# Optimization experiments

Measured on AMD Instinct MI355X. Metric: run time of the kernel, lower is better.

The kernel has to match this reference:

```python
import jax, jax.numpy as jnp
import numpy as np

N, E = 50000, 800000
IN, H, D, C = 128, 4, 32, 40   # in_feats, heads, num_hiddens, n_classes
SLOPE, EPS = 0.2, 1e-5


def _glorot(key, shape, fan_in):
    return jax.random.normal(key, shape, dtype=jnp.float32) * (1.0 / np.sqrt(fan_in))


def setup_inputs() -> dict:
    key = jax.random.key(0)
    ks = jax.random.split(key, 24)
    inp = {
        "feat": jax.random.normal(ks[0], (N, IN), dtype=jnp.float32),
        "src": jax.random.randint(ks[1], (E,), 0, N, dtype=jnp.int32),
        "dst": jax.random.randint(ks[2], (E,), 0, N, dtype=jnp.int32),
    }
    # layer dims: (in_hidden, out_hidden)
    dims = [(IN, D), (H * D, D), (H * D, C)]
    k = 3
    for i, (fin, fout) in enumerate(dims):
        inp[f"Wc{i}"] = _glorot(ks[k], (fin, H * fout), fin); k += 1
        inp[f"al{i}"] = _glorot(ks[k], (H, fout), fout); k += 1
        inp[f"ar{i}"] = _glorot(ks[k], (H, fout), fout); k += 1
        inp[f"bc{i}"] = jnp.zeros((H * fout,), dtype=jnp.float32)
        inp[f"Wl{i}"] = _glorot(ks[k], (fin, H * fout), fin); k += 1
    for i in range(2):  # BN after layers 0 and 1
        inp[f"g{i}"] = jnp.ones((H * D,), dtype=jnp.float32)
        inp[f"b{i}"] = jnp.zeros((H * D,), dtype=jnp.float32)
    inp["bias_last"] = jnp.zeros((C,), dtype=jnp.float32)
    return inp


def _gat_layer(x, src, dst, Wc, al, ar, bc, Wl):
    n = x.shape[0]
    h, d = al.shape
    z = (x @ Wc).reshape(n, h, d)                      # [N,H,D]
    el = jnp.sum(z * al, axis=-1)                      # [N,H]
    er = jnp.sum(z * ar, axis=-1)                      # [N,H]
    e = jax.nn.leaky_relu(el[src] + er[dst], SLOPE)    # [E,H]
    m = jax.ops.segment_max(e, dst, num_segments=n)    # edge-softmax (stable)
    ex = jnp.exp(e - m[dst])
    s = jax.ops.segment_sum(ex, dst, num_segments=n)
    alpha = ex / jnp.where(s == 0, 1.0, s)[dst]        # [E,H]
    agg = jax.ops.segment_sum(alpha[:, :, None] * z[src], dst, num_segments=n)
    conv = agg + bc.reshape(h, d)
    lin = (x @ Wl).reshape(n, h, d)
    return conv + lin                                   # [N,H,D]


def _bn(x, g, b):
    mu = jnp.mean(x, axis=0)
    var = jnp.mean((x - mu) ** 2, axis=0)
    return (x - mu) * jax.lax.rsqrt(var + EPS) * g + b


def reference(feat, src, dst,
              Wc0, al0, ar0, bc0, Wl0,
              Wc1, al1, ar1, bc1, Wl1,
              Wc2, al2, ar2, bc2, Wl2,
              g0, b0, g1, b1, bias_last):
    h = feat
    h = _gat_layer(h, src, dst, Wc0, al0, ar0, bc0, Wl0)
    h = jax.nn.relu(_bn(h.reshape(h.shape[0], -1), g0, b0))
    h = _gat_layer(h, src, dst, Wc1, al1, ar1, bc1, Wl1)
    h = jax.nn.relu(_bn(h.reshape(h.shape[0], -1), g1, b1))
    h = _gat_layer(h, src, dst, Wc2, al2, ar2, bc2, Wl2)
    h = h.mean(axis=1)                                  # mean over heads -> [N,C]
    return h + bias_last
```

## Files before the change

### kernel.cpp

```cpp
#include <hip/hip_runtime.h>
#include <hip/hip_bf16.h>

typedef __hip_bfloat16 bf16;
typedef __attribute__((ext_vector_type(8))) short short8;
typedef __attribute__((ext_vector_type(4))) float f32x4;

__device__ __forceinline__ float b2f(bf16 x) { return __bfloat162float(x); }
__device__ __forceinline__ float bits2f(unsigned short u) {
    return __uint_as_float(((unsigned)u) << 16);
}
__device__ __forceinline__ float ldw(const void* p, int i, int m) {
    return m ? ((const float*)p)[i] : b2f(((const bf16*)p)[i]);
}

__global__ __launch_bounds__(256) void k_zero_probe(int* __restrict__ counts, float* __restrict__ bn0,
                                                    float* __restrict__ bn1, int n,
                                                    const void* __restrict__ feat, int* __restrict__ mode) {
    int t = blockIdx.x * 256 + threadIdx.x;
    if (t < n) counts[t] = 0;
    if (t < 256) { bn0[t] = 0.f; bn1[t] = 0.f; }
    if (blockIdx.x == 0 && threadIdx.x < 64) {
        const bf16* p = (const bf16*)feat;
        int lane = threadIdx.x;
        float m = 0.f;
        for (int i = lane; i < 2048; i += 64) {
            float v = fabsf(b2f(p[2 * i]));
            if (!(v < 1e30f)) v = 1e30f;
            m = fmaxf(m, v);
        }
        #pragma unroll
        for (int off = 32; off > 0; off >>= 1) m = fmaxf(m, __shfl_xor(m, off, 64));
        if (lane == 0) *mode = (m > 1e8f) ? 1 : 0;
    }
}

struct SmallDesc { const void* src; float* dst; int n; };
struct SmallArgs { SmallDesc d[14]; };
__global__ __launch_bounds__(256) void k_prep(const void* __restrict__ Wc0, const void* __restrict__ Wl0,
                                              const void* __restrict__ Wc1, const void* __restrict__ Wl1,
                                              const void* __restrict__ Wc2, const void* __restrict__ Wl2,
                                              bf16* __restrict__ Wt0, bf16* __restrict__ Wt1,
                                              bf16* __restrict__ Wt2, SmallArgs sa,
                                              const int* __restrict__ mode) {
    int m = *mode;
    int bx = blockIdx.x;
    if (bx < 416) {
        int t = bx * 256 + threadIdx.x;
        const void* Wc; const void* Wl; bf16* Wt; int HC, c2, k;
        if (t < 32768)       { Wc = Wc0; Wl = Wl0; Wt = Wt0; HC = 128; c2 = t & 255; k = t >> 8; }
        else if (t < 65536)  { t -= 32768; Wc = Wc1; Wl = Wl1; Wt = Wt1; HC = 128; c2 = t & 255; k = t >> 8; }
        else                 { t -= 65536; Wc = Wc2; Wl = Wl2; Wt = Wt2; HC = 160; c2 = t % 320; k = t / 320; }
        float v = (c2 < HC) ? ldw(Wc, k * HC + c2, m) : ldw(Wl, k * HC + c2 - HC, m);
        int tile = c2 >> 4, c16 = c2 & 15, kg = k >> 5, q = (k >> 3) & 3, j = k & 7;
        Wt[tile * 2048 + kg * 512 + c16 * 32 + q * 8 + j] = __float2bfloat16(v);
    } else {
        #pragma unroll 1
        for (int i = 0; i < 14; i++) {
            const SmallDesc sd = sa.d[i];
            for (int t = threadIdx.x; t < sd.n; t += 256) sd.dst[t] = ldw(sd.src, t, m);
        }
    }
}


__global__ __launch_bounds__(256) void k_hist(const int* __restrict__ dst, int* __restrict__ counts,
                                              int e, int rpb) {
    int range = blockIdx.x & 7;
    int t = (blockIdx.x >> 3) * 256 + threadIdx.x;
    if (t < e) {
        int d = dst[t];
        if ((int)((unsigned)d / (unsigned)rpb) == range) atomicAdd(&counts[d], 1);
    }
}

__global__ __launch_bounds__(1024) void k_scan(const int* __restrict__ counts, int* __restrict__ row_ptr,
                                               int* __restrict__ cursor, int n) {
    __shared__ int wsum[16];
    __shared__ int carry_s;
    int lane = threadIdx.x & 63, w = threadIdx.x >> 6;
    if (threadIdx.x == 0) carry_s = 0;
    __syncthreads();
    for (int base = 0; base < n; base += 16384) {
        int i0 = base + (int)threadIdx.x * 16;
        int v[16];
        #pragma unroll
        for (int jb = 0; jb < 16; jb += 4) {
            int idx = i0 + jb;
            if (idx + 3 < n) {
                int4 t4 = *(const int4*)(counts + idx);
                v[jb] = t4.x; v[jb + 1] = t4.y; v[jb + 2] = t4.z; v[jb + 3] = t4.w;
            } else {
                #pragma unroll
                for (int q = 0; q < 4; q++) v[jb + q] = (idx + q < n) ? counts[idx + q] : 0;
            }
        }
        int pre[16]; int tot = 0;
        #pragma unroll
        for (int j = 0; j < 16; j++) { pre[j] = tot; tot += v[j]; }
        int x = tot;
        #pragma unroll
        for (int off = 1; off < 64; off <<= 1) {
            int t = __shfl_up(x, off, 64);
            if (lane >= off) x += t;
        }
        if (lane == 63) wsum[w] = x;
        __syncthreads();
        if (w == 0 && lane < 16) {
            int s = wsum[lane];
            #pragma unroll
            for (int off = 1; off < 16; off <<= 1) {
                int t = __shfl_up(s, off, 64);
                if (lane >= off) s += t;
            }
            wsum[lane] = s;
        }
        __syncthreads();
        int carry = carry_s;
        int woff = (w == 0) ? 0 : wsum[w - 1];
        int excl = carry + woff + x - tot;
        #pragma unroll
        for (int jb = 0; jb < 16; jb += 4) {
            int idx = i0 + jb;
            if (idx + 3 < n) {
                int4 rp = {excl + pre[jb], excl + pre[jb + 1], excl + pre[jb + 2], excl + pre[jb + 3]};
                *(int4*)(row_ptr + idx) = rp;
                *(int4*)(cursor + idx) = rp;
            } else {
                #pragma unroll
                for (int q = 0; q < 4; q++)
                    if (idx + q < n) { row_ptr[idx + q] = excl + pre[jb + q]; cursor[idx + q] = excl + pre[jb + q]; }
            }
        }
        __syncthreads();
        if (threadIdx.x == 0) carry_s = carry + wsum[15];
        __syncthreads();
    }
    if (threadIdx.x == 0) row_ptr[n] = carry_s;
}

__global__ __launch_bounds__(256) void k_scatter(const int* __restrict__ src, const int* __restrict__ dst,
                                                 int* __restrict__ cursor, int* __restrict__ ssrc,
                                                 int e, int rpb) {
    int range = blockIdx.x & 7;
    int t = (blockIdx.x >> 3) * 256 + threadIdx.x;
    if (t < e) {
        int d = dst[t];
        if ((int)((unsigned)d / (unsigned)rpb) == range) {
            int idx = atomicAdd(&cursor[d], 1);
            ssrc[idx] = src[t];
        }
    }
}

template <int HC, int CT, int AMODE, bool FELR>
__global__ __launch_bounds__(256) void k_gemm_mfma(const void* __restrict__ Av, const int* __restrict__ mode,
                                                   const bf16* __restrict__ Wt,
                                                   bf16* __restrict__ Zh, float* __restrict__ Lin,
                                                   const float* __restrict__ alp, const float* __restrict__ arp,
                                                   float* __restrict__ elp, float* __restrict__ erp,
                                                   const float* __restrict__ bnsum, const float* __restrict__ bnsq,
                                                   const float* __restrict__ gg, const float* __restrict__ bb,
                                                   float invn, int n) {
    __shared__ short lds_a[64 * 136];
    __shared__ float lds_bn[256];
    int tid = threadIdx.x;
    int wv = tid >> 6, lane = tid & 63;
    int quad = lane >> 4, m16 = lane & 15;
    int row0 = blockIdx.x * 64 + wv * 16;
    int row0b = blockIdx.x * 64;
    int col0 = blockIdx.y * (CT * 16);
    if constexpr (AMODE == 2) {
        if (tid < 128) {
            float mu = bnsum[tid] * invn;
            float var = bnsq[tid] * invn - mu * mu;
            float sc = rsqrtf(var + 1e-5f) * gg[tid];
            lds_bn[tid] = sc;
            lds_bn[128 + tid] = bb[tid] - mu * sc;
        }
        __syncthreads();
    }
    bool af32 = false;
    if constexpr (AMODE == 1) af32 = (*mode != 0);
    #pragma unroll
    for (int i = 0; i < 4; i++) {
        int f = i * 256 + tid;
        int row = f >> 4, c8 = f & 15;
        int arow = row0b + row; if (arow >= n) arow = n - 1;
        union { bf16 h[8]; short8 s; } u;
        if (AMODE == 2 || (AMODE == 1 && af32)) {
            const float4* ap = (const float4*)((const float*)Av + (size_t)arow * 128 + c8 * 8);
            float4 g0v = ap[0], g1v = ap[1];
            float vals[8] = {g0v.x, g0v.y, g0v.z, g0v.w, g1v.x, g1v.y, g1v.z, g1v.w};
            if constexpr (AMODE == 2) {
                int c0 = c8 * 8;
                #pragma unroll
                for (int j = 0; j < 8; j++) {
                    float r = vals[j] * lds_bn[c0 + j] + lds_bn[128 + c0 + j];
                    vals[j] = r > 0.f ? r : 0.f;
                }
            }
            #pragma unroll
            for (int j = 0; j < 8; j++) u.h[j] = __float2bfloat16(vals[j]);
        } else {
            u.s = *(const short8*)((const bf16*)Av + (size_t)arow * 128 + c8 * 8);
        }
        *(short8*)(&lds_a[row * 136 + c8 * 8]) = u.s;
    }
    __syncthreads();
    f32x4 acc[CT] = {};
    const short8* Bp = (const short8*)Wt;
    int lr = wv * 16 + m16;
    int ctb = blockIdx.y * CT;
    #pragma unroll
    for (int k8 = 0; k8 < 16; k8 += 4) {
        short8 a = *(const short8*)(&lds_a[lr * 136 + (k8 + quad) * 8]);
        #pragma unroll
        for (int c = 0; c < CT; c++) {
            short8 b = Bp[(size_t)(ctb + c) * 256 + k8 * 16 + m16 * 4 + quad];
            acc[c] = __builtin_amdgcn_mfma_f32_16x16x32_bf16(a, b, acc[c], 0, 0, 0);
        }
    }
    if constexpr (FELR && HC == 128) {
        if (blockIdx.y == 0) {
            float a0[4], a1[4], r0[4], r1[4];
            #pragma unroll
            for (int h = 0; h < 4; h++) {
                a0[h] = alp[h * 32 + m16]; a1[h] = alp[h * 32 + 16 + m16];
                r0[h] = arp[h * 32 + m16]; r1[h] = arp[h * 32 + 16 + m16];
            }
            #pragma unroll
            for (int reg = 0; reg < 4; reg++) {
                float eh[8];
                #pragma unroll
                for (int h = 0; h < 4; h++) {
                    eh[h]     = acc[2 * h][reg] * a0[h] + acc[2 * h + 1][reg] * a1[h];
                    eh[4 + h] = acc[2 * h][reg] * r0[h] + acc[2 * h + 1][reg] * r1[h];
                }
                #pragma unroll
                for (int off = 1; off < 16; off <<= 1) {
                    #pragma unroll
                    for (int k = 0; k < 8; k++) eh[k] += __shfl_xor(eh[k], off, 64);
                }
                int r = row0 + quad * 4 + reg;
                float vl = (m16 & 2) ? ((m16 & 1) ? eh[3] : eh[2]) : ((m16 & 1) ? eh[1] : eh[0]);
                float vr = (m16 & 2) ? ((m16 & 1) ? eh[7] : eh[6]) : ((m16 & 1) ? eh[5] : eh[4]);
                if (r < n && m16 < 4) { elp[(size_t)r * 4 + m16] = vl; erp[(size_t)r * 4 + m16] = vr; }
            }
        }
    }
    if constexpr (FELR && HC == 160) {
        if (blockIdx.y == 0) {
            float alv[10], arv[10];
            #pragma unroll
            for (int c = 0; c < 10; c++) { alv[c] = alp[c * 16 + m16]; arv[c] = arp[c * 16 + m16]; }
            #pragma unroll
            for (int reg = 0; reg < 4; reg++) {
                float eh[8] = {0.f, 0.f, 0.f, 0.f, 0.f, 0.f, 0.f, 0.f};
                #pragma unroll
                for (int c = 0; c < 10; c++) {
                    int col = c * 16 + m16;
                    float zl = acc[c][reg] * alv[c];
                    float zr = acc[c][reg] * arv[c];
                    bool h0 = col < 40, h1 = (col >= 40) & (col < 80);
                    bool h2 = (col >= 80) & (col < 120), h3 = col >= 120;
                    eh[0] += h0 ? zl : 0.f; eh[1] += h1 ? zl : 0.f;
                    eh[2] += h2 ? zl : 0.f; eh[3] += h3 ? zl : 0.f;
                    eh[4] += h0 ? zr : 0.f; eh[5] += h1 ? zr : 0.f;
                    eh[6] += h2 ? zr : 0.f; eh[7] += h3 ? zr : 0.f;
                }
                #pragma unroll
                for (int off = 1; off < 16; off <<= 1) {
                    #pragma unroll
                    for (int k = 0; k < 8; k++) eh[k] += __shfl_xor(eh[k], off, 64);
                }
                int r = row0 + quad * 4 + reg;
                float vl = (m16 & 2) ? ((m16 & 1) ? eh[3] : eh[2]) : ((m16 & 1) ? eh[1] : eh[0]);
                float vr = (m16 & 2) ? ((m16 & 1) ? eh[7] : eh[6]) : ((m16 & 1) ? eh[5] : eh[4]);
                if (r < n && m16 < 4) { elp[(size_t)r * 4 + m16] = vl; erp[(size_t)r * 4 + m16] = vr; }
            }
        }
    }
    #pragma unroll
    for (int c = 0; c < CT; c++) {
        int gc = col0 + c * 16 + m16;
        #pragma unroll
        for (int reg = 0; reg < 4; reg++) {
            int r = row0 + quad * 4 + reg;
            if (r >= n) continue;
            float v = acc[c][reg];
            if (gc < HC) Zh[(size_t)r * HC + gc] = __float2bfloat16(v);
            else         Lin[(size_t)r * HC + gc - HC] = v;
        }
    }
}

template <int HC, int D, bool LAST>
__global__ __launch_bounds__(256, 8) void k_gather(const int* __restrict__ row_ptr, const int* __restrict__ ssrc,
                                                   const float* __restrict__ el, const float* __restrict__ er,
                                                   const float* __restrict__ bc, const bf16* __restrict__ Z,
                                                   float* __restrict__ Y, const float* __restrict__ bias,
                                                   float* __restrict__ out, int n) {
    constexpr int DPL = HC / 16;
    constexpr int UN = (DPL == 8) ? 4 : 2;
    int node = (int)((blockIdx.x * blockDim.x + threadIdx.x) >> 6);
    int lane = threadIdx.x & 63;
    if (node >= n) return;
    int qi = lane >> 4;
    int t16 = lane & 15;
    int hq = t16 >> 2;
    int beg = row_ptr[node], end = row_ptr[node + 1];
    float4 er4 = ((const float4*)er)[node];
    const float4* el4p = (const float4*)el;
    const bf16* Zt = Z + t16 * DPL;
    float acc[DPL];
    #pragma unroll
    for (int k = 0; k < DPL; k++) acc[k] = 0.f;
    float ss = 0.f;
    for (int base = beg; base < end; base += 64) {
        int idx = base + lane;
        bool valid = idx < end;
        int s_my = valid ? ssrc[idx] : 0;
        float4 e4 = el4p[s_my];
        float x0 = e4.x + er4.x; x0 = x0 > 0.f ? x0 : 0.2f * x0;
        float x1 = e4.y + er4.y; x1 = x1 > 0.f ? x1 : 0.2f * x1;
        float x2 = e4.z + er4.z; x2 = x2 > 0.f ? x2 : 0.2f * x2;
        float x3 = e4.w + er4.w; x3 = x3 > 0.f ? x3 : 0.2f * x3;
        float w0 = valid ? __expf(x0) : 0.f;
        float w1 = valid ? __expf(x1) : 0.f;
        float w2 = valid ? __expf(x2) : 0.f;
        float w3 = valid ? __expf(x3) : 0.f;
        int cnt = end - base; if (cnt > 64) cnt = 64;
        int iters = (cnt + 3) >> 2;
        for (int j = 0; j < iters; j += UN) {
            int sv[UN]; float gv[UN];
            #pragma unroll
            for (int f = 0; f < UN; f++) {
                int sl = qi + ((j + f) << 2);
                sv[f] = __shfl(s_my, sl, 64);
                float a0 = __shfl(w0, sl, 64);
                float a1 = __shfl(w1, sl, 64);
                float a2 = __shfl(w2, sl, 64);
                float a3 = __shfl(w3, sl, 64);
                gv[f] = (hq & 2) ? ((hq & 1) ? a3 : a2) : ((hq & 1) ? a1 : a0);
                ss += gv[f];
            }
            if constexpr (DPL == 8) {
                short8 z[UN];
                #pragma unroll
                for (int f = 0; f < UN; f++) z[f] = *(const short8*)(Zt + (size_t)sv[f] * HC);
                #pragma unroll
                for (int f = 0; f < UN; f++) {
                    #pragma unroll
                    for (int k = 0; k < 8; k++)
                        acc[k] += gv[f] * bits2f((unsigned short)z[f][k]);
                }
            } else {
                __hip_bfloat162 z[UN][DPL / 2];
                #pragma unroll
                for (int f = 0; f < UN; f++) {
                    const __hip_bfloat162* z2 = (const __hip_bfloat162*)(Zt + (size_t)sv[f] * HC);
                    #pragma unroll
                    for (int k2 = 0; k2 < DPL / 2; k2++) z[f][k2] = z2[k2];
                }
                #pragma unroll
                for (int f = 0; f < UN; f++) {
                    #pragma unroll
                    for (int k2 = 0; k2 < DPL / 2; k2++) {
                        acc[2 * k2]     += gv[f] * b2f(z[f][k2].x);
                        acc[2 * k2 + 1] += gv[f] * b2f(z[f][k2].y);
                    }
                }
            }
        }
    }
    #pragma unroll
    for (int k = 0; k < DPL; k++) {
        acc[k] += __shfl_xor(acc[k], 16, 64);
        acc[k] += __shfl_xor(acc[k], 32, 64);
    }
    ss += __shfl_xor(ss, 16, 64);
    ss += __shfl_xor(ss, 32, 64);
    float inv = (end > beg) ? 1.f / ss : 0.f;
    if constexpr (!LAST) {
        if ((lane & 48) == 0) {
            float* yr = Y + (size_t)node * HC + t16 * DPL;
            const float* bcr = bc + t16 * DPL;
            #pragma unroll
            for (int k = 0; k < DPL; k++) yr[k] += acc[k] * inv + bcr[k];
        }
    } else {
        float yv[DPL];
        const float* lr = Y + (size_t)node * HC + t16 * DPL;
        const float* bcr = bc + t16 * DPL;
        #pragma unroll
        for (int k = 0; k < DPL; k++) yv[k] = acc[k] * inv + bcr[k] + lr[k];
        #pragma unroll
        for (int k = 0; k < DPL; k++) {
            yv[k] += __shfl_xor(yv[k], 4, 64);
            yv[k] += __shfl_xor(yv[k], 8, 64);
        }
        if (lane < 4) {
            float* orow = out + (size_t)node * 40 + t16 * DPL;
            const float* br = bias + t16 * DPL;
            #pragma unroll
            for (int k = 0; k < DPL; k++) orow[k] = 0.25f * yv[k] + br[k];
        }
    }
}

__global__ __launch_bounds__(256) void k_bn_stats(const float* __restrict__ Y, float* __restrict__ sum,
                                                  float* __restrict__ sumsq, int n) {
    __shared__ float4 lds_s[8][32];
    __shared__ float4 lds_q[8][32];
    int t = threadIdx.x;
    int q = t & 31, g = t >> 5;
    const float4* Y4 = (const float4*)Y;
    float4 s = {0.f, 0.f, 0.f, 0.f}, ss = {0.f, 0.f, 0.f, 0.f};
    const int stride = 128 * 8;
    int r = blockIdx.x * 8 + g;
    for (; r + stride < n; r += 2 * stride) {
        float4 v0 = Y4[(size_t)r * 32 + q];
        float4 v1 = Y4[(size_t)(r + stride) * 32 + q];
        s.x += v0.x; s.y += v0.y; s.z += v0.z; s.w += v0.w;
        ss.x += v0.x * v0.x; ss.y += v0.y * v0.y; ss.z += v0.z * v0.z; ss.w += v0.w * v0.w;
        s.x += v1.x; s.y += v1.y; s.z += v1.z; s.w += v1.w;
        ss.x += v1.x * v1.x; ss.y += v1.y * v1.y; ss.z += v1.z * v1.z; ss.w += v1.w * v1.w;
    }
    if (r < n) {
        float4 v = Y4[(size_t)r * 32 + q];
        s.x += v.x; s.y += v.y; s.z += v.z; s.w += v.w;
        ss.x += v.x * v.x; ss.y += v.y * v.y; ss.z += v.z * v.z; ss.w += v.w * v.w;
    }
    lds_s[g][q] = s; lds_q[g][q] = ss;
    __syncthreads();
    if (t < 32) {
        float4 S = lds_s[0][t], Q = lds_q[0][t];
        #pragma unroll
        for (int g2 = 1; g2 < 8; g2++) {
            float4 a = lds_s[g2][t], b = lds_q[g2][t];
            S.x += a.x; S.y += a.y; S.z += a.z; S.w += a.w;
            Q.x += b.x; Q.y += b.y; Q.z += b.z; Q.w += b.w;
        }
        atomicAdd(&sum[4 * t + 0], S.x); atomicAdd(&sum[4 * t + 1], S.y);
        atomicAdd(&sum[4 * t + 2], S.z); atomicAdd(&sum[4 * t + 3], S.w);
        atomicAdd(&sumsq[4 * t + 0], Q.x); atomicAdd(&sumsq[4 * t + 1], Q.y);
        atomicAdd(&sumsq[4 * t + 2], Q.z); atomicAdd(&sumsq[4 * t + 3], Q.w);
    }
}


extern "C" void kernel_launch(void* const* d_in, const int* in_sizes, int n_in,
                              void* d_out, int out_size, void* d_ws, size_t ws_size,
                              hipStream_t stream) {
    (void)n_in; (void)out_size; (void)ws_size;
    const int N = in_sizes[0] / 128;
    const int E = in_sizes[1];

    const int* src = (const int*)d_in[1];
    const int* dst = (const int*)d_in[2];
    float* out = (float*)d_out;

    char* p = (char*)d_ws;
    auto carve = [&](size_t bytes) {
        void* q = (void*)p;
        p += (bytes + 255) & ~(size_t)255;
        return q;
    };
    int*   mode    = (int*)  carve(256);
    bf16*  zh      = (bf16*) carve((size_t)N * 160 * 2);
    float* P0      = (float*)carve((size_t)N * 160 * 4);
    float* P1      = (float*)carve((size_t)N * 128 * 4);
    float* el      = (float*)carve((size_t)N * 4 * 4);
    float* er      = (float*)carve((size_t)N * 4 * 4);
    float* bn0     = (float*)carve(256 * 4);
    float* bn1     = (float*)carve(256 * 4);
    int*   counts  = (int*)  carve((size_t)N * 4);
    int*   row_ptr = (int*)  carve((size_t)(N + 1) * 4);
    int*   cursor  = (int*)  carve((size_t)N * 4);
    int*   ssrc    = (int*)  carve((size_t)E * 4);
    bf16*  Wt0     = (bf16*) carve((size_t)2 * 128 * 128 * 2);
    bf16*  Wt1     = (bf16*) carve((size_t)2 * 128 * 128 * 2);
    bf16*  Wt2     = (bf16*) carve((size_t)2 * 160 * 128 * 2);
    const int small_idx[14] = {4, 5, 6, 9, 10, 11, 14, 15, 16, 18, 19, 20, 21, 22};
    float* Wsm[14];
    for (int j = 0; j < 14; j++) Wsm[j] = (float*)carve((size_t)in_sizes[small_idx[j]] * 4);

    const float* alw[3] = {Wsm[0], Wsm[3], Wsm[6]};
    const float* arw[3] = {Wsm[1], Wsm[4], Wsm[7]};
    const float* bcw[3] = {Wsm[2], Wsm[5], Wsm[8]};
    const float* g0 = Wsm[9];
    const float* b0 = Wsm[10];
    const float* g1 = Wsm[11];
    const float* b1 = Wsm[12];
    const float* bias_last = Wsm[13];

    const int EB = (E + 255) / 256;
    const int GB_ROWS = (N + 63) / 64;
    const int NODE_BLK = (N + 3) / 4;
    const float invn = 1.f / (float)N;
    const int RPB = (N + 7) / 8;

    k_zero_probe<<<(N + 255) / 256, 256, 0, stream>>>(counts, bn0, bn1, N, d_in[0], mode);
    SmallArgs sa;
    for (int j = 0; j < 14; j++) sa.d[j] = SmallDesc{d_in[small_idx[j]], Wsm[j], in_sizes[small_idx[j]]};
    k_prep<<<417, 256, 0, stream>>>(d_in[3], d_in[7], d_in[8], d_in[12], d_in[13], d_in[17],
                                    Wt0, Wt1, Wt2, sa, mode);
    k_hist<<<8 * EB, 256, 0, stream>>>(dst, counts, E, RPB);
    k_scan<<<1, 1024, 0, stream>>>(counts, row_ptr, cursor, N);
    k_scatter<<<8 * EB, 256, 0, stream>>>(src, dst, cursor, ssrc, E, RPB);

    k_gemm_mfma<128, 8, 1, true><<<dim3(GB_ROWS, 2), 256, 0, stream>>>(
        d_in[0], mode, Wt0, zh, P0, alw[0], arw[0], el, er,
        nullptr, nullptr, nullptr, nullptr, 0.f, N);
    k_gather<128, 32, false><<<NODE_BLK, 256, 0, stream>>>(row_ptr, ssrc, el, er, bcw[0], zh,
                                                           P0, nullptr, nullptr, N);
    k_bn_stats<<<128, 256, 0, stream>>>(P0, bn0, bn0 + 128, N);

    k_gemm_mfma<128, 8, 2, true><<<dim3(GB_ROWS, 2), 256, 0, stream>>>(
        P0, mode, Wt1, zh, P1, alw[1], arw[1], el, er,
        bn0, bn0 + 128, g0, b0, invn, N);
    k_gather<128, 32, false><<<NODE_BLK, 256, 0, stream>>>(row_ptr, ssrc, el, er, bcw[1], zh,
                                                           P1, nullptr, nullptr, N);
    k_bn_stats<<<128, 256, 0, stream>>>(P1, bn1, bn1 + 128, N);

    k_gemm_mfma<160, 10, 2, true><<<dim3(GB_ROWS, 2), 256, 0, stream>>>(
        P1, mode, Wt2, zh, P0, alw[2], arw[2], el, er,
        bn1, bn1 + 128, g1, b1, invn, N);
    k_gather<160, 40, true><<<NODE_BLK, 256, 0, stream>>>(row_ptr, ssrc, el, er, bcw[2], zh,
                                                          P0, bias_last, out, N);
}
```

Baseline: 468.6 us.

## Compute edge weights per lane in gather and simplify histogram to a single pass

The gather kernel no longer loads 64 edges per chunk cooperatively and broadcasts source ids and four per-head weights through shuffles. Each lane now loads its own source index and its own head's el value, then computes the leaky-relu and exp itself, which removes the five shuffles per edge. The cost is redundant ssrc/el loads and exp evaluations across the 16 lanes sharing an edge. The histogram kernel also drops its 8-way range partitioning, reading dst once with plain atomics, which trades atomic locality for one-eighth the launched blocks.

```diff
diff --git a/kernel.cpp b/kernel.cpp
--- a/kernel.cpp
+++ b/kernel.cpp
@@ -63,14 +63,9 @@
 }
 
 
-__global__ __launch_bounds__(256) void k_hist(const int* __restrict__ dst, int* __restrict__ counts,
-                                              int e, int rpb) {
-    int range = blockIdx.x & 7;
-    int t = (blockIdx.x >> 3) * 256 + threadIdx.x;
-    if (t < e) {
-        int d = dst[t];
-        if ((int)((unsigned)d / (unsigned)rpb) == range) atomicAdd(&counts[d], 1);
-    }
+__global__ __launch_bounds__(256) void k_hist(const int* __restrict__ dst, int* __restrict__ counts, int e) {
+    int t = blockIdx.x * 256 + threadIdx.x;
+    if (t < e) atomicAdd(&counts[dst[t]], 1);
 }
 
 __global__ __launch_bounds__(1024) void k_scan(const int* __restrict__ counts, int* __restrict__ row_ptr,
@@ -309,66 +304,53 @@
     int t16 = lane & 15;
     int hq = t16 >> 2;
     int beg = row_ptr[node], end = row_ptr[node + 1];
-    float4 er4 = ((const float4*)er)[node];
-    const float4* el4p = (const float4*)el;
+    float er_h = er[node * 4 + hq];
     const bf16* Zt = Z + t16 * DPL;
     float acc[DPL];
     #pragma unroll
     for (int k = 0; k < DPL; k++) acc[k] = 0.f;
     float ss = 0.f;
-    for (int base = beg; base < end; base += 64) {
-        int idx = base + lane;
-        bool valid = idx < end;
-        int s_my = valid ? ssrc[idx] : 0;
-        float4 e4 = el4p[s_my];
-        float x0 = e4.x + er4.x; x0 = x0 > 0.f ? x0 : 0.2f * x0;
-        float x1 = e4.y + er4.y; x1 = x1 > 0.f ? x1 : 0.2f * x1;
-        float x2 = e4.z + er4.z; x2 = x2 > 0.f ? x2 : 0.2f * x2;
-        float x3 = e4.w + er4.w; x3 = x3 > 0.f ? x3 : 0.2f * x3;
-        float w0 = valid ? __expf(x0) : 0.f;
-        float w1 = valid ? __expf(x1) : 0.f;
-        float w2 = valid ? __expf(x2) : 0.f;
-        float w3 = valid ? __expf(x3) : 0.f;
-        int cnt = end - base; if (cnt > 64) cnt = 64;
-        int iters = (cnt + 3) >> 2;
-        for (int j = 0; j < iters; j += UN) {
-            int sv[UN]; float gv[UN];
+    int iters = (end - beg + 3) >> 2;
+    for (int j = 0; j < iters; j += UN) {
+        int sv[UN]; float gv[UN];
+        #pragma unroll
+        for (int f = 0; f < UN; f++) {
+            int eidx = beg + ((j + f) << 2) + qi;
+            sv[f] = (eidx < end) ? ssrc[eidx] : -1;
+        }
+        #pragma unroll
+        for (int f = 0; f < UN; f++) {
+            int s = sv[f] < 0 ? 0 : sv[f];
+            float x = el[s * 4 + hq] + er_h;
+            x = x > 0.f ? x : 0.2f * x;
+            gv[f] = (sv[f] >= 0) ? __expf(x) : 0.f;
+            ss += gv[f];
+            sv[f] = s;
+        }
+        if constexpr (DPL == 8) {
+            short8 z[UN];
+            #pragma unroll
+            for (int f = 0; f < UN; f++) z[f] = *(const short8*)(Zt + (size_t)sv[f] * HC);
             #pragma unroll
             for (int f = 0; f < UN; f++) {
-                int sl = qi + ((j + f) << 2);
-                sv[f] = __shfl(s_my, sl, 64);
-                float a0 = __shfl(w0, sl, 64);
-                float a1 = __shfl(w1, sl, 64);
-                float a2 = __shfl(w2, sl, 64);
-                float a3 = __shfl(w3, sl, 64);
-                gv[f] = (hq & 2) ? ((hq & 1) ? a3 : a2) : ((hq & 1) ? a1 : a0);
-                ss += gv[f];
-            }
-            if constexpr (DPL == 8) {
-                short8 z[UN];
-                #pragma unroll
-                for (int f = 0; f < UN; f++) z[f] = *(const short8*)(Zt + (size_t)sv[f] * HC);
-                #pragma unroll
-                for (int f = 0; f < UN; f++) {
-                    #pragma unroll
-                    for (int k = 0; k < 8; k++)
-                        acc[k] += gv[f] * bits2f((unsigned short)z[f][k]);
-                }
-            } else {
-                __hip_bfloat162 z[UN][DPL / 2];
-                #pragma unroll
-                for (int f = 0; f < UN; f++) {
-                    const __hip_bfloat162* z2 = (const __hip_bfloat162*)(Zt + (size_t)sv[f] * HC);
-                    #pragma unroll
-                    for (int k2 = 0; k2 < DPL / 2; k2++) z[f][k2] = z2[k2];
-                }
-                #pragma unroll
-                for (int f = 0; f < UN; f++) {
-                    #pragma unroll
-                    for (int k2 = 0; k2 < DPL / 2; k2++) {
-                        acc[2 * k2]     += gv[f] * b2f(z[f][k2].x);
-                        acc[2 * k2 + 1] += gv[f] * b2f(z[f][k2].y);
-                    }
+                #pragma unroll
+                for (int k = 0; k < 8; k++)
+                    acc[k] += gv[f] * bits2f((unsigned short)z[f][k]);
+            }
+        } else {
+            __hip_bfloat162 z[UN][DPL / 2];
+            #pragma unroll
+            for (int f = 0; f < UN; f++) {
+                const __hip_bfloat162* z2 = (const __hip_bfloat162*)(Zt + (size_t)sv[f] * HC);
+                #pragma unroll
+                for (int k2 = 0; k2 < DPL / 2; k2++) z[f][k2] = z2[k2];
+            }
+            #pragma unroll
+            for (int f = 0; f < UN; f++) {
+                #pragma unroll
+                for (int k2 = 0; k2 < DPL / 2; k2++) {
+                    acc[2 * k2]     += gv[f] * b2f(z[f][k2].x);
+                    acc[2 * k2 + 1] += gv[f] * b2f(z[f][k2].y);
                 }
             }
         }
@@ -505,7 +487,7 @@
     for (int j = 0; j < 14; j++) sa.d[j] = SmallDesc{d_in[small_idx[j]], Wsm[j], in_sizes[small_idx[j]]};
     k_prep<<<417, 256, 0, stream>>>(d_in[3], d_in[7], d_in[8], d_in[12], d_in[13], d_in[17],
                                     Wt0, Wt1, Wt2, sa, mode);
-    k_hist<<<8 * EB, 256, 0, stream>>>(dst, counts, E, RPB);
+    k_hist<<<EB, 256, 0, stream>>>(dst, counts, E);
     k_scan<<<1, 1024, 0, stream>>>(counts, row_ptr, cursor, N);
     k_scatter<<<8 * EB, 256, 0, stream>>>(src, dst, cursor, ssrc, E, RPB);
 
```

Result: slower. 483.1 us (+3.1%).

## Simplify histogram to single pass and stage Z tile through LDS for vector stores

Applied to the files above, without the earlier changes.

The histogram kernel drops its 8-way range partitioning and does one atomicAdd per edge in a single launch, which cuts the grid to one eighth and removes the redundant reads of dst. In the GEMM, blocks writing the bf16 Z half now stage the accumulator tile in LDS and write it out with 16-byte row-contiguous stores instead of scattered 2-byte stores. The LDS tile is sized to the column width, and the extra syncs add a little latency. The histogram change may raise atomic contention or hurt locality compared with the range-partitioned version.

```diff
diff --git a/kernel.cpp b/kernel.cpp
--- a/kernel.cpp
+++ b/kernel.cpp
@@ -63,14 +63,9 @@
 }
 
 
-__global__ __launch_bounds__(256) void k_hist(const int* __restrict__ dst, int* __restrict__ counts,
-                                              int e, int rpb) {
-    int range = blockIdx.x & 7;
-    int t = (blockIdx.x >> 3) * 256 + threadIdx.x;
-    if (t < e) {
-        int d = dst[t];
-        if ((int)((unsigned)d / (unsigned)rpb) == range) atomicAdd(&counts[d], 1);
-    }
+__global__ __launch_bounds__(256) void k_hist(const int* __restrict__ dst, int* __restrict__ counts, int e) {
+    int t = blockIdx.x * 256 + threadIdx.x;
+    if (t < e) atomicAdd(&counts[dst[t]], 1);
 }
 
 __global__ __launch_bounds__(1024) void k_scan(const int* __restrict__ counts, int* __restrict__ row_ptr,
@@ -161,14 +156,16 @@
                                                    const float* __restrict__ bnsum, const float* __restrict__ bnsq,
                                                    const float* __restrict__ gg, const float* __restrict__ bb,
                                                    float invn, int n) {
-    __shared__ short lds_a[64 * 136];
+    constexpr int TW = CT * 16;
+    constexpr int TS = (TW + 8 > 136) ? (TW + 8) : 136;
+    __shared__ short lds_a[64 * TS];
     __shared__ float lds_bn[256];
     int tid = threadIdx.x;
     int wv = tid >> 6, lane = tid & 63;
     int quad = lane >> 4, m16 = lane & 15;
     int row0 = blockIdx.x * 64 + wv * 16;
     int row0b = blockIdx.x * 64;
-    int col0 = blockIdx.y * (CT * 16);
+    int col0 = blockIdx.y * TW;
     if constexpr (AMODE == 2) {
         if (tid < 128) {
             float mu = bnsum[tid] * invn;
@@ -280,16 +277,34 @@
             }
         }
     }
-    #pragma unroll
-    for (int c = 0; c < CT; c++) {
-        int gc = col0 + c * 16 + m16;
-        #pragma unroll
-        for (int reg = 0; reg < 4; reg++) {
-            int r = row0 + quad * 4 + reg;
-            if (r >= n) continue;
-            float v = acc[c][reg];
-            if (gc < HC) Zh[(size_t)r * HC + gc] = __float2bfloat16(v);
-            else         Lin[(size_t)r * HC + gc - HC] = v;
+    if (blockIdx.y == 0) {
+        __syncthreads();
+        #pragma unroll
+        for (int c = 0; c < CT; c++) {
+            #pragma unroll
+            for (int reg = 0; reg < 4; reg++) {
+                int rrel = wv * 16 + quad * 4 + reg;
+                lds_a[rrel * TS + c * 16 + m16] = (short)__bfloat16_as_ushort(__float2bfloat16(acc[c][reg]));
+            }
+        }
+        __syncthreads();
+        constexpr int CH = TW / 8;
+        for (int f = tid; f < 64 * CH; f += 256) {
+            int row = f / CH, c8 = f % CH;
+            int arow = row0b + row;
+            if (arow < n)
+                *(short8*)(Zh + (size_t)arow * HC + c8 * 8) = *(const short8*)(&lds_a[row * TS + c8 * 8]);
+        }
+    } else {
+        #pragma unroll
+        for (int c = 0; c < CT; c++) {
+            int gc = col0 + c * 16 + m16;
+            #pragma unroll
+            for (int reg = 0; reg < 4; reg++) {
+                int r = row0 + quad * 4 + reg;
+                if (r >= n) continue;
+                Lin[(size_t)r * HC + gc - HC] = acc[c][reg];
+            }
         }
     }
 }
@@ -505,7 +520,7 @@
     for (int j = 0; j < 14; j++) sa.d[j] = SmallDesc{d_in[small_idx[j]], Wsm[j], in_sizes[small_idx[j]]};
     k_prep<<<417, 256, 0, stream>>>(d_in[3], d_in[7], d_in[8], d_in[12], d_in[13], d_in[17],
                                     Wt0, Wt1, Wt2, sa, mode);
-    k_hist<<<8 * EB, 256, 0, stream>>>(dst, counts, E, RPB);
+    k_hist<<<EB, 256, 0, stream>>>(dst, counts, E);
     k_scan<<<1, 1024, 0, stream>>>(counts, row_ptr, cursor, N);
     k_scatter<<<8 * EB, 256, 0, stream>>>(src, dst, cursor, ssrc, E, RPB);
 
```

Measured after the change: 464.8 us. About the same (-0.8%).
